# Optimization experiments

Hardware: AMD Instinct MI355X
Metric: run time of the kernel (lower is better)

Reference implementation:

```python
import jax, jax.numpy as jnp
import numpy as np

S, B, H = 2048, 2, 2048
NH = 16
HD = H // NH
SCALE = HD ** -0.5


def setup_inputs() -> dict:
    key = jax.random.key(0)
    ks = jax.random.split(key, 5)
    sigma = 0.02
    return {
        "x": jax.random.normal(ks[0], (S, B, H), dtype=jnp.float32),
        "wq": jax.random.normal(ks[1], (H, H), dtype=jnp.float32) * sigma,
        "wk": jax.random.normal(ks[2], (H, H), dtype=jnp.float32) * sigma,
        "wv": jax.random.normal(ks[3], (H, H), dtype=jnp.float32) * sigma,
        "wo": jax.random.normal(ks[4], (H, H), dtype=jnp.float32) * sigma,
    }


def reference(x, wq, wk, wv, wo):
    # x: [s, b, h]; F.linear(x, W) == x @ W.T
    q = x @ wq.T
    k = x @ wk.T
    v = x @ wv.T
    s, b, _ = q.shape
    # [s, b, h] -> [b, nh, s, hd]
    def split_heads(t):
        return t.reshape(s, b, NH, HD).transpose(1, 2, 0, 3)
    q, k, v = split_heads(q), split_heads(k), split_heads(v)
    scores = jnp.einsum("bhqd,bhkd->bhqk", q, k) * SCALE
    attn = jax.nn.softmax(scores.astype(jnp.float32), axis=-1).astype(q.dtype)
    out = jnp.einsum("bhqk,bhkd->bhqd", attn, v)
    # [b, nh, s, hd] -> [s, b, h]
    out = out.transpose(2, 0, 1, 3).reshape(s, b, NH * HD)
    return out @ wo.T
```

## Files before the change

kernel.cpp:

```cpp
#include <hip/hip_runtime.h>

typedef __bf16 bf16;
typedef __bf16 bf16x8 __attribute__((ext_vector_type(8)));
typedef float f32x4 __attribute__((ext_vector_type(4)));
typedef float f32x16 __attribute__((ext_vector_type(16)));
typedef unsigned int uint;
typedef uint uint2v __attribute__((ext_vector_type(2)));

#define GLOAD16(g, l)                                                        \
  __builtin_amdgcn_global_load_lds(                                          \
      (const __attribute__((address_space(1))) void*)(g),                    \
      (__attribute__((address_space(3))) void*)(l), 16, 0, 0)

__device__ inline uint pack_bf16(float a, float b) {
  union { bf16 h[2]; uint u; } x;
  x.h[0] = (bf16)a; x.h[1] = (bf16)b;
  return x.u;
}

__global__ void cast_f32_to_bf16(const float* __restrict__ in,
                                 bf16* __restrict__ out, int n8, float scale) {
  int i = blockIdx.x * blockDim.x + threadIdx.x;
  if (i >= n8) return;
  const float4* p = reinterpret_cast<const float4*>(in) + (size_t)i * 2;
  float4 a = p[0], b = p[1];
  bf16x8 o;
  o[0] = (bf16)(a.x * scale); o[1] = (bf16)(a.y * scale);
  o[2] = (bf16)(a.z * scale); o[3] = (bf16)(a.w * scale);
  o[4] = (bf16)(b.x * scale); o[5] = (bf16)(b.y * scale);
  o[6] = (bf16)(b.z * scale); o[7] = (bf16)(b.w * scale);
  *reinterpret_cast<bf16x8*>(out + (size_t)i * 8) = o;
}

template <typename OT>
__global__ __launch_bounds__(512, 2) void gemm_nt_256(
    const bf16* __restrict__ A, const bf16* __restrict__ B, OT* __restrict__ C,
    int K, int lda, int ldb, int ldc, long bsB, long bsC) {
  extern __shared__ char sh[];
  const int t = threadIdx.x;
  const int w = t >> 6, lane = t & 63;
  const int l15 = lane & 15, l4 = lane >> 4;
  const int wr = w >> 1, wc = w & 1;
  const int gx = gridDim.x, gy = gridDim.y;
  const int nwg = gx * gy;
  const int bid = blockIdx.y * gx + blockIdx.x;
  const int fid = (bid & 7) * (nwg >> 3) + (bid >> 3);
  const int by = fid / gx, bx = fid - by * gx;
  const int m0 = by * 256;
  const int n0 = bx * 128;
  const bf16* Bg = B + (size_t)blockIdx.z * bsB;
  OT* Cg = C + (size_t)blockIdx.z * bsC;

  int sRow[4], sCol[4];
#pragma unroll
  for (int i = 0; i < 4; i++) {
    int sB_ = (i * 512 + t) * 16;
    int row = sB_ >> 7;
    int ge = (sB_ ^ ((row & 7) << 4)) >> 1;
    sRow[i] = ge >> 6;
    sCol[i] = ge & 63;
  }

  const int NT = K >> 6;
  f32x4 acc[4][4] = {};

  auto stage = [&](int tt) {
    char* dst = sh + (size_t)(tt % 3) * 49152;
    const int k0 = tt * 64;
#pragma unroll
    for (int i = 0; i < 4; i++)
      GLOAD16(A + (size_t)(m0 + sRow[i]) * lda + k0 + sCol[i],
              dst + (i * 512 + w * 64) * 16);
#pragma unroll
    for (int i = 0; i < 2; i++)
      GLOAD16(Bg + (size_t)(n0 + sRow[i]) * ldb + k0 + sCol[i],
              dst + 32768 + (i * 512 + w * 64) * 16);
  };

  stage(0);
  stage(1);
  for (int tt = 0; tt < NT; ++tt) {
    if (tt < NT - 1)
      asm volatile("s_waitcnt vmcnt(6)" ::: "memory");
    else
      asm volatile("s_waitcnt vmcnt(0)" ::: "memory");
    __builtin_amdgcn_s_barrier();

    const char* Ab = sh + (size_t)(tt % 3) * 49152;
    const char* Bb = Ab + 32768;
    bf16x8 bfr[4][2];
#pragma unroll
    for (int n = 0; n < 4; n++)
#pragma unroll
      for (int kk = 0; kk < 2; kk++) {
        int row = wc * 64 + n * 16 + l15;
        int off = (row * 128 + kk * 64 + l4 * 16) ^ ((row & 7) << 4);
        bfr[n][kk] = *reinterpret_cast<const bf16x8*>(Bb + off);
      }
    bf16x8 af0[2][2];
#pragma unroll
    for (int m = 0; m < 2; m++)
#pragma unroll
      for (int kk = 0; kk < 2; kk++) {
        int row = wr * 64 + m * 16 + l15;
        int off = (row * 128 + kk * 64 + l4 * 16) ^ ((row & 7) << 4);
        af0[m][kk] = *reinterpret_cast<const bf16x8*>(Ab + off);
      }
    __builtin_amdgcn_s_setprio(1);
#pragma unroll
    for (int m = 0; m < 2; m++)
#pragma unroll
      for (int n = 0; n < 4; n++)
#pragma unroll
        for (int kk = 0; kk < 2; kk++)
          acc[m][n] = __builtin_amdgcn_mfma_f32_16x16x32_bf16(
              af0[m][kk], bfr[n][kk], acc[m][n], 0, 0, 0);
    __builtin_amdgcn_s_setprio(0);

    if (tt + 2 < NT) stage(tt + 2);

    bf16x8 af1[2][2];
#pragma unroll
    for (int m = 0; m < 2; m++)
#pragma unroll
      for (int kk = 0; kk < 2; kk++) {
        int row = wr * 64 + (2 + m) * 16 + l15;
        int off = (row * 128 + kk * 64 + l4 * 16) ^ ((row & 7) << 4);
        af1[m][kk] = *reinterpret_cast<const bf16x8*>(Ab + off);
      }
    __builtin_amdgcn_s_setprio(1);
#pragma unroll
    for (int m = 0; m < 2; m++)
#pragma unroll
      for (int n = 0; n < 4; n++)
#pragma unroll
        for (int kk = 0; kk < 2; kk++)
          acc[2 + m][n] = __builtin_amdgcn_mfma_f32_16x16x32_bf16(
              af1[m][kk], bfr[n][kk], acc[2 + m][n], 0, 0, 0);
    __builtin_amdgcn_s_setprio(0);
  }

#pragma unroll
  for (int m = 0; m < 4; m++)
#pragma unroll
    for (int n = 0; n < 4; n++)
#pragma unroll
      for (int j = 0; j < 4; j++) {
        int row = m0 + wr * 64 + m * 16 + l4 * 4 + j;
        int col = n0 + wc * 64 + n * 16 + l15;
        Cg[(size_t)row * ldc + col] = (OT)acc[m][n][j];
      }
}

__global__ __launch_bounds__(256, 2) void attn_fwd(
    const bf16* __restrict__ Q, const bf16* __restrict__ Kb,
    const bf16* __restrict__ Vt, bf16* __restrict__ O) {
  __shared__ bf16 Ks[2][64 * 128];
  __shared__ bf16 Vs[2][64 * 128];
  const int t = threadIdx.x, w = t >> 6, lane = t & 63;
  const int l31 = lane & 31, half = lane >> 5;
  const int bh = blockIdx.x;
  const int b = bh >> 4, h = bh & 15;
  const int sq0 = blockIdx.y * 128 + w * 32;
  const size_t hoff = (size_t)h * 128;
  const size_t bO = (size_t)b * 2048 + hoff;

  bf16x8 qf[8];
  {
    const bf16* qp = Q + ((size_t)(sq0 + l31) * 2 + b) * 2048 + hoff + half * 8;
#pragma unroll
    for (int dc = 0; dc < 8; dc++)
      qf[dc] = *reinterpret_cast<const bf16x8*>(qp + dc * 16);
  }

  const bf16* kp[4];
  const bf16* vp[4];
#pragma unroll
  for (int i = 0; i < 4; i++) {
    int s = i * 256 + t;
    int row = s >> 4, g = s & 15;
    int lg = g ^ (row & 15);
    kp[i] = Kb + ((size_t)row * 2 + b) * 2048 + hoff + lg * 8;
    int d = row * 2 + (lg >> 3);
    vp[i] = Vt + (bO + d) * 2048 + (lg & 7) * 8;
  }

  auto stage = [&](int nb, int sk0) {
#pragma unroll
    for (int i = 0; i < 4; i++)
      GLOAD16(kp[i] + (size_t)sk0 * 4096, Ks[nb] + (i * 256 + w * 64) * 8);
#pragma unroll
    for (int i = 0; i < 4; i++)
      GLOAD16(vp[i] + sk0, Vs[nb] + (i * 256 + w * 64) * 8);
  };

  f32x16 acc_o[4] = {};
  float m_run = -3e38f, l_run = 0.f;

  stage(0, 0);

  for (int it = 0; it < 32; ++it) {
    const int cur = it & 1;
    __syncthreads();

    const char* ksb = reinterpret_cast<const char*>(Ks[cur]);
    const char* vsb = reinterpret_cast<const char*>(Vs[cur]);

    f32x16 sc[2] = {};
    __builtin_amdgcn_s_setprio(1);
#pragma unroll
    for (int dc = 0; dc < 8; dc++) {
      int kx = ((dc * 2 + half) ^ (l31 & 15)) << 4;
#pragma unroll
      for (int kt = 0; kt < 2; kt++) {
        int kB = ((kt * 32 + l31) << 8) + kx;
        bf16x8 kf = *reinterpret_cast<const bf16x8*>(ksb + kB);
        sc[kt] = __builtin_amdgcn_mfma_f32_32x32x16_bf16(kf, qf[dc], sc[kt], 0, 0, 0);
      }
    }
    __builtin_amdgcn_s_setprio(0);

    if (it + 1 < 32) stage(cur ^ 1, (it + 1) * 64);

    float red[8];
#pragma unroll
    for (int r = 0; r < 8; r++)
      red[r] = fmaxf(fmaxf(sc[0][r], sc[0][r + 8]),
                     fmaxf(sc[1][r], sc[1][r + 8]));
#pragma unroll
    for (int s = 4; s >= 1; s >>= 1)
#pragma unroll
      for (int r = 0; r < s; r++) red[r] = fmaxf(red[r], red[r + s]);
    float pmax = fmaxf(red[0], __shfl_xor(red[0], 32));

    if (!__all(pmax - m_run <= 11.0f)) {
      float mn = fmaxf(m_run, pmax);
      float f = exp2f(m_run - mn);
      m_run = mn;
      l_run *= f;
#pragma unroll
      for (int idx = 0; idx < 16; idx++) {
        float fr = __shfl(f, (idx & 3) + 8 * (idx >> 2) + half * 4);
#pragma unroll
        for (int dcb = 0; dcb < 4; dcb++) acc_o[dcb][idx] *= fr;
      }
    }

#pragma unroll
    for (int kt = 0; kt < 2; kt++)
#pragma unroll
      for (int r = 0; r < 16; r++) sc[kt][r] = exp2f(sc[kt][r] - m_run);
#pragma unroll
    for (int r = 0; r < 8; r++)
      red[r] = (sc[0][r] + sc[0][r + 8]) + (sc[1][r] + sc[1][r + 8]);
#pragma unroll
    for (int s = 4; s >= 1; s >>= 1)
#pragma unroll
      for (int r = 0; r < s; r++) red[r] += red[r + s];
    l_run += red[0] + __shfl_xor(red[0], 32);

    uint pa[4][4];
#pragma unroll
    for (int skc = 0; skc < 4; skc++) {
      int kt = skc >> 1, s8 = (skc & 1) * 8;
      uint pk01 = pack_bf16(sc[kt][s8 + 0], sc[kt][s8 + 1]);
      uint pk23 = pack_bf16(sc[kt][s8 + 2], sc[kt][s8 + 3]);
      uint pk45 = pack_bf16(sc[kt][s8 + 4], sc[kt][s8 + 5]);
      uint pk67 = pack_bf16(sc[kt][s8 + 6], sc[kt][s8 + 7]);
      uint2v r02 = __builtin_amdgcn_permlane32_swap(pk01, pk45, false, false);
      uint2v r13 = __builtin_amdgcn_permlane32_swap(pk23, pk67, false, false);
      pa[skc][0] = r02[0];
      pa[skc][1] = r13[0];
      pa[skc][2] = r02[1];
      pa[skc][3] = r13[1];
    }

    __builtin_amdgcn_s_setprio(1);
#pragma unroll
    for (int dcb = 0; dcb < 4; dcb++) {
      int rp = dcb * 16 + (l31 >> 1);
      int pbit = (l31 & 1) << 3;
#pragma unroll
      for (int skc = 0; skc < 4; skc++) {
        int vB = (rp << 8) + (((pbit + skc * 2 + half) ^ (l31 >> 1)) << 4);
        bf16x8 vf = *reinterpret_cast<const bf16x8*>(vsb + vB);
        union { uint u[4]; bf16x8 v; } af;
        af.u[0] = pa[skc][0]; af.u[1] = pa[skc][1];
        af.u[2] = pa[skc][2]; af.u[3] = pa[skc][3];
        acc_o[dcb] = __builtin_amdgcn_mfma_f32_32x32x16_bf16(
            af.v, vf, acc_o[dcb], 0, 0, 0);
      }
    }
    __builtin_amdgcn_s_setprio(0);
  }

  float inv = 1.0f / l_run;
#pragma unroll
  for (int idx = 0; idx < 16; idx++) {
    int sr = (idx & 3) + 8 * (idx >> 2) + half * 4;
    float invr = __shfl(inv, sr);
    bf16* op = O + ((size_t)(sq0 + sr) * 2 + b) * 2048 + hoff + l31;
#pragma unroll
    for (int dcb = 0; dcb < 4; dcb++)
      op[dcb * 32] = (bf16)(acc_o[dcb][idx] * invr);
  }
}

extern "C" void kernel_launch(void* const* d_in, const int* in_sizes, int n_in,
                              void* d_out, int out_size, void* d_ws,
                              size_t ws_size, hipStream_t stream) {
  (void)in_sizes; (void)n_in; (void)out_size; (void)ws_size;
  const float* x  = (const float*)d_in[0];
  const float* wq = (const float*)d_in[1];
  const float* wk = (const float*)d_in[2];
  const float* wv = (const float*)d_in[3];
  const float* wo = (const float*)d_in[4];
  float* out = (float*)d_out;
  char* ws = (char*)d_ws;
  bf16* xb   = (bf16*)(ws);
  bf16* qb   = (bf16*)(ws + (1u << 24));
  bf16* kb   = (bf16*)(ws + (2u << 24));
  bf16* vt   = (bf16*)(ws + (3u << 24));
  bf16* wb   = (bf16*)(ws + (4u << 24));
  bf16* attn = xb;
  const float SCALE = 0.08838834764831845f * 1.4426950408889634f;
  const int SMEM = 3 * 49152;

  hipFuncSetAttribute((const void*)gemm_nt_256<bf16>,
                      hipFuncAttributeMaxDynamicSharedMemorySize, SMEM);
  hipFuncSetAttribute((const void*)gemm_nt_256<float>,
                      hipFuncAttributeMaxDynamicSharedMemorySize, SMEM);

  cast_f32_to_bf16<<<4096, 256, 0, stream>>>(x, xb, 8388608 / 8, 1.0f);

  dim3 g1(16, 16, 1);
  cast_f32_to_bf16<<<2048, 256, 0, stream>>>(wq, wb, 4194304 / 8, SCALE);
  gemm_nt_256<bf16><<<g1, 512, SMEM, stream>>>(xb, wb, qb, 2048, 2048, 2048, 2048, 0, 0);

  cast_f32_to_bf16<<<2048, 256, 0, stream>>>(wk, wb, 4194304 / 8, 1.0f);
  gemm_nt_256<bf16><<<g1, 512, SMEM, stream>>>(xb, wb, kb, 2048, 2048, 2048, 2048, 0, 0);

  cast_f32_to_bf16<<<2048, 256, 0, stream>>>(wv, wb, 4194304 / 8, 1.0f);
  dim3 g2(16, 8, 2);
  gemm_nt_256<bf16><<<g2, 512, SMEM, stream>>>(wb, xb, vt, 2048, 2048, 4096, 2048,
                                               2048L, 4194304L);

  dim3 ga(32, 16);
  attn_fwd<<<ga, 256, 0, stream>>>(qb, kb, vt, attn);

  cast_f32_to_bf16<<<2048, 256, 0, stream>>>(wo, wb, 4194304 / 8, 1.0f);
  gemm_nt_256<float><<<g1, 512, SMEM, stream>>>(attn, wb, out, 2048, 2048, 2048, 2048, 0, 0);
}
```

Before: 270.2 us.

## Fuse Q/K projections into one GEMM and triple-buffer attention K/V loads

The Q and K projection weights are cast into one contiguous buffer and multiplied in a single GEMM launch with twice the N-tiles. Output columns past 2048 are redirected to the K buffer through a split offset. The attention kernel moves to 512-thread blocks covering 256 queries each, with a three-slot dynamic-shared-memory ring that prefetches two tiles ahead. It waits on vmcnt instead of a full sync before each barrier. This aims to cut launch count, improve GEMM occupancy and overlap K/V loads with compute, at the cost of more LDS per block and hand-tuned waitcnt logic.

Result: no change. 271.5 us (+0.5%).

```diff
diff --git a/kernel.cpp b/kernel.cpp
--- a/kernel.cpp
+++ b/kernel.cpp
@@ -35,7 +35,7 @@
 template <typename OT>
 __global__ __launch_bounds__(512, 2) void gemm_nt_256(
     const bf16* __restrict__ A, const bf16* __restrict__ B, OT* __restrict__ C,
-    int K, int lda, int ldb, int ldc, long bsB, long bsC) {
+    int K, int lda, int ldb, int ldc, long bsB, long bsC, long cSplit) {
   extern __shared__ char sh[];
   const int t = threadIdx.x;
   const int w = t >> 6, lane = t & 63;
@@ -49,7 +49,7 @@
   const int m0 = by * 256;
   const int n0 = bx * 128;
   const bf16* Bg = B + (size_t)blockIdx.z * bsB;
-  OT* Cg = C + (size_t)blockIdx.z * bsC;
+  OT* Cg = C + (size_t)blockIdx.z * bsC + ((n0 & 2048) ? cSplit : 0);
 
   int sRow[4], sCol[4];
 #pragma unroll
@@ -152,16 +152,15 @@
       }
 }
 
-__global__ __launch_bounds__(256, 2) void attn_fwd(
+__global__ __launch_bounds__(512, 2) void attn_fwd(
     const bf16* __restrict__ Q, const bf16* __restrict__ Kb,
     const bf16* __restrict__ Vt, bf16* __restrict__ O) {
-  __shared__ bf16 Ks[2][64 * 128];
-  __shared__ bf16 Vs[2][64 * 128];
+  extern __shared__ char ash[];
   const int t = threadIdx.x, w = t >> 6, lane = t & 63;
   const int l31 = lane & 31, half = lane >> 5;
   const int bh = blockIdx.x;
   const int b = bh >> 4, h = bh & 15;
-  const int sq0 = blockIdx.y * 128 + w * 32;
+  const int sq0 = blockIdx.y * 256 + w * 32;
   const size_t hoff = (size_t)h * 128;
   const size_t bO = (size_t)b * 2048 + hoff;
 
@@ -173,11 +172,11 @@
       qf[dc] = *reinterpret_cast<const bf16x8*>(qp + dc * 16);
   }
 
-  const bf16* kp[4];
-  const bf16* vp[4];
-#pragma unroll
-  for (int i = 0; i < 4; i++) {
-    int s = i * 256 + t;
+  const bf16* kp[2];
+  const bf16* vp[2];
+#pragma unroll
+  for (int i = 0; i < 2; i++) {
+    int s = i * 512 + t;
     int row = s >> 4, g = s & 15;
     int lg = g ^ (row & 15);
     kp[i] = Kb + ((size_t)row * 2 + b) * 2048 + hoff + lg * 8;
@@ -185,26 +184,32 @@
     vp[i] = Vt + (bO + d) * 2048 + (lg & 7) * 8;
   }
 
-  auto stage = [&](int nb, int sk0) {
-#pragma unroll
-    for (int i = 0; i < 4; i++)
-      GLOAD16(kp[i] + (size_t)sk0 * 4096, Ks[nb] + (i * 256 + w * 64) * 8);
-#pragma unroll
-    for (int i = 0; i < 4; i++)
-      GLOAD16(vp[i] + sk0, Vs[nb] + (i * 256 + w * 64) * 8);
+  auto stage = [&](int slot, int sk0) {
+    char* Kd = ash + (size_t)slot * 32768;
+    char* Vd = Kd + 16384;
+#pragma unroll
+    for (int i = 0; i < 2; i++)
+      GLOAD16(kp[i] + (size_t)sk0 * 4096, Kd + (i * 512 + w * 64) * 16);
+#pragma unroll
+    for (int i = 0; i < 2; i++)
+      GLOAD16(vp[i] + sk0, Vd + (i * 512 + w * 64) * 16);
   };
 
   f32x16 acc_o[4] = {};
   float m_run = -3e38f, l_run = 0.f;
 
   stage(0, 0);
+  stage(1, 64);
 
   for (int it = 0; it < 32; ++it) {
-    const int cur = it & 1;
-    __syncthreads();
-
-    const char* ksb = reinterpret_cast<const char*>(Ks[cur]);
-    const char* vsb = reinterpret_cast<const char*>(Vs[cur]);
+    if (it < 31)
+      asm volatile("s_waitcnt vmcnt(4)" ::: "memory");
+    else
+      asm volatile("s_waitcnt vmcnt(0)" ::: "memory");
+    __builtin_amdgcn_s_barrier();
+
+    const char* ksb = ash + (size_t)(it % 3) * 32768;
+    const char* vsb = ksb + 16384;
 
     f32x16 sc[2] = {};
     __builtin_amdgcn_s_setprio(1);
@@ -220,7 +225,7 @@
     }
     __builtin_amdgcn_s_setprio(0);
 
-    if (it + 1 < 32) stage(cur ^ 1, (it + 1) * 64);
+    if (it + 2 < 32) stage((it + 2) % 3, (it + 2) * 64);
 
     float red[8];
 #pragma unroll
@@ -322,32 +327,38 @@
   bf16* kb   = (bf16*)(ws + (2u << 24));
   bf16* vt   = (bf16*)(ws + (3u << 24));
   bf16* wb   = (bf16*)(ws + (4u << 24));
+  bf16* wqk  = vt;
   bf16* attn = xb;
   const float SCALE = 0.08838834764831845f * 1.4426950408889634f;
   const int SMEM = 3 * 49152;
+  const int SMEM_A = 3 * 32768;
+  const long CSPLIT = (long)(kb - qb) - 2048;
 
   hipFuncSetAttribute((const void*)gemm_nt_256<bf16>,
                       hipFuncAttributeMaxDynamicSharedMemorySize, SMEM);
   hipFuncSetAttribute((const void*)gemm_nt_256<float>,
                       hipFuncAttributeMaxDynamicSharedMemorySize, SMEM);
+  hipFuncSetAttribute((const void*)attn_fwd,
+                      hipFuncAttributeMaxDynamicSharedMemorySize, SMEM_A);
 
   cast_f32_to_bf16<<<4096, 256, 0, stream>>>(x, xb, 8388608 / 8, 1.0f);
 
-  dim3 g1(16, 16, 1);
-  cast_f32_to_bf16<<<2048, 256, 0, stream>>>(wq, wb, 4194304 / 8, SCALE);
-  gemm_nt_256<bf16><<<g1, 512, SMEM, stream>>>(xb, wb, qb, 2048, 2048, 2048, 2048, 0, 0);
-
-  cast_f32_to_bf16<<<2048, 256, 0, stream>>>(wk, wb, 4194304 / 8, 1.0f);
-  gemm_nt_256<bf16><<<g1, 512, SMEM, stream>>>(xb, wb, kb, 2048, 2048, 2048, 2048, 0, 0);
+  cast_f32_to_bf16<<<2048, 256, 0, stream>>>(wq, wqk, 4194304 / 8, SCALE);
+  cast_f32_to_bf16<<<2048, 256, 0, stream>>>(wk, wqk + 4194304, 4194304 / 8, 1.0f);
+  dim3 gqk(32, 16, 1);
+  gemm_nt_256<bf16><<<gqk, 512, SMEM, stream>>>(xb, wqk, qb, 2048, 2048, 2048,
+                                                2048, 0, 0, CSPLIT);
 
   cast_f32_to_bf16<<<2048, 256, 0, stream>>>(wv, wb, 4194304 / 8, 1.0f);
   dim3 g2(16, 8, 2);
   gemm_nt_256<bf16><<<g2, 512, SMEM, stream>>>(wb, xb, vt, 2048, 2048, 4096, 2048,
-                                               2048L, 4194304L);
-
-  dim3 ga(32, 16);
-  attn_fwd<<<ga, 256, 0, stream>>>(qb, kb, vt, attn);
+                                               2048L, 4194304L, 0);
+
+  dim3 ga(32, 8);
+  attn_fwd<<<ga, 512, SMEM_A, stream>>>(qb, kb, vt, attn);
 
   cast_f32_to_bf16<<<2048, 256, 0, stream>>>(wo, wb, 4194304 / 8, 1.0f);
-  gemm_nt_256<float><<<g1, 512, SMEM, stream>>>(attn, wb, out, 2048, 2048, 2048, 2048, 0, 0);
-}
+  dim3 g1(16, 16, 1);
+  gemm_nt_256<float><<<g1, 512, SMEM, stream>>>(attn, wb, out, 2048, 2048, 2048,
+                                                2048, 0, 0, 0);
+}
```
